# Optimization experiments

Hardware: AMD Instinct MI355X
Metric: run time of the kernel (lower is better)

## Reference

```python
import jax, jax.numpy as jnp
import numpy as np

N, NB = 256, 8732  # batch, default boxes (SSD300)


def setup_inputs() -> dict:
    key = jax.random.key(0)
    k1, k2, k3, k4, k5 = jax.random.split(key, 5)
    ploc = jax.random.normal(k1, (N, 4, NB), dtype=jnp.float32)
    plabel = jax.random.normal(k2, (N, 1, NB), dtype=jnp.float32)
    # gloc / dboxes need strictly positive w,h (log / division); offset uniform
    gloc = jax.random.uniform(k3, (N, 4, NB), dtype=jnp.float32) + 0.1
    glabel = jax.random.randint(k4, (N, NB), 0, 2).astype(jnp.int64)
    dboxes = jax.random.uniform(k5, (1, 4, NB), dtype=jnp.float32) + 0.1
    return {"ploc": ploc, "plabel": plabel, "gloc": gloc,
            "glabel": glabel, "dboxes": dboxes}


def _bce_logits(x, y):
    # numerically stable BCEWithLogits, reduction='none'
    return jnp.maximum(x, 0.0) - x * y + jnp.log1p(jnp.exp(-jnp.abs(x)))


def _smooth_l1(d):
    ad = jnp.abs(d)
    return jnp.where(ad < 1.0, 0.5 * d * d, ad - 0.5)


def reference(ploc, plabel, gloc, glabel, dboxes):
    scale_xy = 1.0
    scale_wh = 1.0
    mask = glabel > 0                              # [N, NB] bool
    pos_num = mask.sum(axis=1)                     # [N] int

    # location target vector
    gxy = scale_xy * (gloc[:, :2, :] - dboxes[:, :2, :]) / dboxes[:, 2:, :]
    gwh = scale_wh * jnp.log(gloc[:, 2:, :] / dboxes[:, 2:, :])
    vec_gd = jnp.concatenate((gxy, gwh), axis=1)   # [N, 4, NB]

    sl1 = _smooth_l1(ploc - vec_gd).sum(axis=1)    # [N, NB]
    sl1 = (mask.astype(sl1.dtype) * sl1).sum(axis=1)  # [N]

    pl = plabel.squeeze(1).astype(jnp.float32)     # [N, NB]
    gl = glabel.astype(jnp.float32)
    con = _bce_logits(pl, gl)                      # [N, NB]

    # hard negative mining: rank negatives by loss, keep top 3*pos_num
    con_neg = jnp.where(mask, 0.0, con)
    con_idx = jnp.argsort(-con_neg, axis=1)        # descending sort indices
    con_rank = jnp.argsort(con_idx, axis=1)        # rank of each position
    neg_num = jnp.clip(3 * pos_num, None, NB)[:, None]
    neg_mask = con_rank < neg_num                  # [N, NB] bool

    keep = (mask | neg_mask).astype(con.dtype)
    closs = (con * keep).sum(axis=1)               # [N]

    total_loss = sl1 + closs
    num_mask = (pos_num > 0).astype(total_loss.dtype)
    pos_f = jnp.clip(pos_num.astype(total_loss.dtype), 1e-6, None)
    return (total_loss * num_mask / pos_f).mean(axis=0)
```

## Files before the change

### kernel.cpp

```cpp
#include <hip/hip_runtime.h>
#include <math.h>

#define N_ROWS 256
#define NB 8732
#define NB4 2183
#define CHUNKS 8
#define TAILN (NB4 - CHUNKS * 256)

typedef float f4 __attribute__((ext_vector_type(4)));
typedef int   i4 __attribute__((ext_vector_type(4)));

__device__ __forceinline__ float smooth_l1(float d) {
    float ad = fabsf(d);
    return ad < 1.0f ? 0.5f * d * d : ad - 0.5f;
}

__device__ __forceinline__ float bce_y0(float x) {
    return fmaxf(x, 0.0f) + log1pf(expf(-fabsf(x)));
}

struct Batch {
    f4 p0, p1, p2, p3, q0, q1, q2, q3, d0, d1, d2, d3, px;
    i4 lb;
};

__device__ __forceinline__ Batch loadB(
    const f4* __restrict__ ploc4, const f4* __restrict__ gloc4,
    const f4* __restrict__ db4, const f4* __restrict__ pl4,
    const i4* __restrict__ gl4, int rb, int rs, int g) {
    Batch b;
    b.p0 = ploc4[rb + 0 * NB4 + g];
    b.p1 = ploc4[rb + 1 * NB4 + g];
    b.p2 = ploc4[rb + 2 * NB4 + g];
    b.p3 = ploc4[rb + 3 * NB4 + g];
    b.q0 = gloc4[rb + 0 * NB4 + g];
    b.q1 = gloc4[rb + 1 * NB4 + g];
    b.q2 = gloc4[rb + 2 * NB4 + g];
    b.q3 = gloc4[rb + 3 * NB4 + g];
    b.d0 = db4[0 * NB4 + g];
    b.d1 = db4[1 * NB4 + g];
    b.d2 = db4[2 * NB4 + g];
    b.d3 = db4[3 * NB4 + g];
    b.lb = gl4[rs + g];
    b.px = pl4[rs + g];
    return b;
}

__device__ __forceinline__ void accumB(const Batch& b, float& sl1, float& cAll,
                                       float& cPos, float& pCnt) {
#pragma unroll
    for (int k = 0; k < 4; ++k) {
        float rw2 = __builtin_amdgcn_rcpf(b.d2[k]);
        float rw3 = __builtin_amdgcn_rcpf(b.d3[k]);
        float gx = (b.q0[k] - b.d0[k]) * rw2;
        float gy = (b.q1[k] - b.d1[k]) * rw3;
        float gw = __logf(b.q2[k] * rw2);
        float gh = __logf(b.q3[k] * rw3);
        float s = smooth_l1(b.p0[k] - gx)
                + smooth_l1(b.p1[k] - gy)
                + smooth_l1(b.p2[k] - gw)
                + smooth_l1(b.p3[k] - gh);
        int lab = b.lb[k];
        float x = b.px[k];
        float con = fmaxf(x, 0.0f) - x * (float)lab
                  + __logf(1.0f + __expf(-fabsf(x)));
        cAll += con;
        float m = (lab > 0) ? 1.0f : 0.0f;
        pCnt += m;
        sl1 += m * s;
        cPos += m * con;
    }
}

__global__ __launch_bounds__(256) void partial_kernel(
    const float* __restrict__ ploc, const float* __restrict__ plabel,
    const float* __restrict__ gloc, const int* __restrict__ glabel,
    const float* __restrict__ dboxes, float* __restrict__ ws) {
    const int row = blockIdx.x;
    const int chunk = blockIdx.y;
    const int tid = threadIdx.x;
    const int g = chunk * 256 + tid;

    const f4* __restrict__ ploc4 = (const f4*)ploc;
    const f4* __restrict__ gloc4 = (const f4*)gloc;
    const f4* __restrict__ db4   = (const f4*)dboxes;
    const f4* __restrict__ pl4   = (const f4*)plabel;
    const i4* __restrict__ gl4   = (const i4*)glabel;

    const int rb = row * 4 * NB4;
    const int rs = row * NB4;

    float sl1acc = 0.0f, conAll = 0.0f, conPos = 0.0f, posCnt = 0.0f;

    {
        Batch b = loadB(ploc4, gloc4, db4, pl4, gl4, rb, rs, g);
        accumB(b, sl1acc, conAll, conPos, posCnt);
    }
    if (chunk == CHUNKS - 1 && tid < TAILN) {
        Batch b = loadB(ploc4, gloc4, db4, pl4, gl4, rb, rs, CHUNKS * 256 + tid);
        accumB(b, sl1acc, conAll, conPos, posCnt);
    }

    float v0 = sl1acc, v1 = conAll, v2 = conPos, v3 = posCnt;
#pragma unroll
    for (int off = 32; off > 0; off >>= 1) {
        v0 += __shfl_down(v0, off);
        v1 += __shfl_down(v1, off);
        v2 += __shfl_down(v2, off);
        v3 += __shfl_down(v3, off);
    }
    __shared__ float sm[4][4];
    const int wid = tid >> 6, lane = tid & 63;
    if (lane == 0) {
        sm[wid][0] = v0; sm[wid][1] = v1; sm[wid][2] = v2; sm[wid][3] = v3;
    }
    __syncthreads();
    if (tid == 0) {
        f4 part;
        part.x = sm[0][0] + sm[1][0] + sm[2][0] + sm[3][0];
        part.y = sm[0][1] + sm[1][1] + sm[2][1] + sm[3][1];
        part.z = sm[0][2] + sm[1][2] + sm[2][2] + sm[3][2];
        part.w = sm[0][3] + sm[1][3] + sm[2][3] + sm[3][3];
        ((f4*)ws)[chunk * N_ROWS + row] = part;
    }
}

__global__ __launch_bounds__(256) void final_kernel(
    const float* __restrict__ ws, const float* __restrict__ plabel,
    const int* __restrict__ glabel, float* __restrict__ out) {
    const int r = threadIdx.x;
    float sl1 = 0.f, cAll = 0.f, cPos = 0.f, posf = 0.f;
#pragma unroll
    for (int c = 0; c < CHUNKS; ++c) {
        f4 p = ((const f4*)ws)[c * N_ROWS + r];
        sl1 += p.x; cAll += p.y; cPos += p.z; posf += p.w;
    }
    const int pos = (int)(posf + 0.5f);
    const long long K = 3LL * (long long)pos;

    float closs;
    if (pos == 0) {
        closs = 0.0f;
    } else if (K >= (long long)NB) {
        closs = cAll;
    } else {
        const int Ki = (int)K;
        const float* plRow = plabel + r * NB;
        const int* glRow = glabel + r * NB;
        unsigned cur = 0;
        for (int bit = 31; bit >= 0; --bit) {
            unsigned trial = cur | (1u << bit);
            int c2 = 0;
            for (int j = 0; j < NB; ++j) {
                if (glRow[j] > 0) continue;
                float con = bce_y0(plRow[j]);
                if (__float_as_uint(con) >= trial) c2++;
            }
            if (c2 >= Ki) cur = trial;
        }
        const float thr = __uint_as_float(cur);
        int cntG = 0; float sumG = 0.f;
        for (int j = 0; j < NB; ++j) {
            if (glRow[j] > 0) continue;
            float con = bce_y0(plRow[j]);
            if (con > thr) { cntG++; sumG += con; }
        }
        closs = cPos + sumG + (float)(Ki - cntG) * thr;
    }

    float loss = (pos > 0) ? (sl1 + closs) / (float)pos : 0.0f;

#pragma unroll
    for (int off = 32; off > 0; off >>= 1) loss += __shfl_down(loss, off);
    __shared__ float sm[4];
    const int wid = threadIdx.x >> 6, lane = threadIdx.x & 63;
    if (lane == 0) sm[wid] = loss;
    __syncthreads();
    if (threadIdx.x == 0) {
        out[0] = (sm[0] + sm[1] + sm[2] + sm[3]) * (1.0f / 256.0f);
    }
}

extern "C" void kernel_launch(void* const* d_in, const int* in_sizes, int n_in,
                              void* d_out, int out_size, void* d_ws, size_t ws_size,
                              hipStream_t stream) {
    const float* ploc   = (const float*)d_in[0];
    const float* plabel = (const float*)d_in[1];
    const float* gloc   = (const float*)d_in[2];
    const int*   glabel = (const int*)d_in[3];
    const float* dboxes = (const float*)d_in[4];
    float* ws  = (float*)d_ws;
    float* out = (float*)d_out;

    dim3 grid(N_ROWS, CHUNKS);
    hipLaunchKernelGGL(partial_kernel, grid, dim3(256), 0, stream,
                       ploc, plabel, gloc, glabel, dboxes, ws);
    hipLaunchKernelGGL(final_kernel, dim3(1), dim3(256), 0, stream,
                       ws, plabel, glabel, out);
}
```

Measured before the change: 22.85 us.

## Fuse partial and final kernels via last-block-done atomics per row

Replaces the two-kernel scheme with a single kernel where blocks atomically accumulate per-row partials and the last-arriving block for each row performs the hard-negative threshold search and adds the row loss to a global accumulator. A global counter elects the final writer of the output. This removes the second launch and the serialized single-block tail. It adds a workspace memset and relies on atomic ordering with explicit waitcnt for correctness.

```diff
diff --git a/kernel.cpp b/kernel.cpp
--- a/kernel.cpp
+++ b/kernel.cpp
@@ -6,6 +6,8 @@
 #define NB4 2183
 #define CHUNKS 8
 #define TAILN (NB4 - CHUNKS * 256)
+#define SLOT_F 32
+#define WS_BYTES ((N_ROWS + 1) * 128)
 
 typedef float f4 __attribute__((ext_vector_type(4)));
 typedef int   i4 __attribute__((ext_vector_type(4)));
@@ -72,10 +74,11 @@
     }
 }
 
-__global__ __launch_bounds__(256) void partial_kernel(
+__global__ __launch_bounds__(256) void fused_kernel(
     const float* __restrict__ ploc, const float* __restrict__ plabel,
     const float* __restrict__ gloc, const int* __restrict__ glabel,
-    const float* __restrict__ dboxes, float* __restrict__ ws) {
+    const float* __restrict__ dboxes, float* __restrict__ ws,
+    float* __restrict__ out) {
     const int row = blockIdx.x;
     const int chunk = blockIdx.y;
     const int tid = threadIdx.x;
@@ -115,29 +118,33 @@
         sm[wid][0] = v0; sm[wid][1] = v1; sm[wid][2] = v2; sm[wid][3] = v3;
     }
     __syncthreads();
-    if (tid == 0) {
-        f4 part;
-        part.x = sm[0][0] + sm[1][0] + sm[2][0] + sm[3][0];
-        part.y = sm[0][1] + sm[1][1] + sm[2][1] + sm[3][1];
-        part.z = sm[0][2] + sm[1][2] + sm[2][2] + sm[3][2];
-        part.w = sm[0][3] + sm[1][3] + sm[2][3] + sm[3][3];
-        ((f4*)ws)[chunk * N_ROWS + row] = part;
-    }
-}
-
-__global__ __launch_bounds__(256) void final_kernel(
-    const float* __restrict__ ws, const float* __restrict__ plabel,
-    const int* __restrict__ glabel, float* __restrict__ out) {
-    const int r = threadIdx.x;
-    float sl1 = 0.f, cAll = 0.f, cPos = 0.f, posf = 0.f;
-#pragma unroll
-    for (int c = 0; c < CHUNKS; ++c) {
-        f4 p = ((const f4*)ws)[c * N_ROWS + r];
-        sl1 += p.x; cAll += p.y; cPos += p.z; posf += p.w;
-    }
+    if (wid != 0) return;
+
+    float* slot = ws + row * SLOT_F;
+    unsigned* rowcnt = (unsigned*)(slot + 4);
+    float* gacc = ws + N_ROWS * SLOT_F;
+    unsigned* gcnt = (unsigned*)(gacc + 4);
+
+    if (lane < 4) {
+        float v = sm[0][lane] + sm[1][lane] + sm[2][lane] + sm[3][lane];
+        atomicAdd(&slot[lane], v);
+    }
+    asm volatile("s_waitcnt vmcnt(0)" ::: "memory");
+    unsigned arr = 0u;
+    if (lane == 0) arr = atomicAdd(rowcnt, 1u);
+    arr = __shfl(arr, 0);
+    if (arr != CHUNKS - 1) return;
+
+    float rv = 0.0f;
+    if (lane < 4) rv = atomicAdd(&slot[lane], 0.0f);
+    float sl1  = __shfl(rv, 0);
+    float cAll = __shfl(rv, 1);
+    float cPos = __shfl(rv, 2);
+    float posf = __shfl(rv, 3);
+    if (lane != 0) return;
+
     const int pos = (int)(posf + 0.5f);
     const long long K = 3LL * (long long)pos;
-
     float closs;
     if (pos == 0) {
         closs = 0.0f;
@@ -145,8 +152,8 @@
         closs = cAll;
     } else {
         const int Ki = (int)K;
-        const float* plRow = plabel + r * NB;
-        const int* glRow = glabel + r * NB;
+        const float* plRow = plabel + row * NB;
+        const int* glRow = glabel + row * NB;
         unsigned cur = 0;
         for (int bit = 31; bit >= 0; --bit) {
             unsigned trial = cur | (1u << bit);
@@ -167,17 +174,13 @@
         }
         closs = cPos + sumG + (float)(Ki - cntG) * thr;
     }
-
     float loss = (pos > 0) ? (sl1 + closs) / (float)pos : 0.0f;
 
-#pragma unroll
-    for (int off = 32; off > 0; off >>= 1) loss += __shfl_down(loss, off);
-    __shared__ float sm[4];
-    const int wid = threadIdx.x >> 6, lane = threadIdx.x & 63;
-    if (lane == 0) sm[wid] = loss;
-    __syncthreads();
-    if (threadIdx.x == 0) {
-        out[0] = (sm[0] + sm[1] + sm[2] + sm[3]) * (1.0f / 256.0f);
+    atomicAdd(gacc, loss * (1.0f / 256.0f));
+    asm volatile("s_waitcnt vmcnt(0)" ::: "memory");
+    unsigned g2 = atomicAdd(gcnt, 1u);
+    if (g2 == N_ROWS - 1) {
+        out[0] = atomicAdd(gacc, 0.0f);
     }
 }
 
@@ -192,9 +195,9 @@
     float* ws  = (float*)d_ws;
     float* out = (float*)d_out;
 
+    hipMemsetAsync(ws, 0, WS_BYTES, stream);
+
     dim3 grid(N_ROWS, CHUNKS);
-    hipLaunchKernelGGL(partial_kernel, grid, dim3(256), 0, stream,
-                       ploc, plabel, gloc, glabel, dboxes, ws);
-    hipLaunchKernelGGL(final_kernel, dim3(1), dim3(256), 0, stream,
-                       ws, plabel, glabel, out);
-}
+    hipLaunchKernelGGL(fused_kernel, grid, dim3(256), 0, stream,
+                       ploc, plabel, gloc, glabel, dboxes, ws, out);
+}
```

After: 31.16 us. 1.36x slower.
